# Kernel tuning notes

Measured on AMD Instinct MI355X. Metric: run time of the kernel, lower is better.

## Reference

```python
import jax, jax.numpy as jnp
import numpy as np

C = 16        # channel_n
HID = 128     # hidden width of 1x1 MLP
FIRE_RATE = 0.5
STEP_SIZE = 1.0
ALIVE_THRESH = 0.1
B, H, W = 16, 256, 256


def _perceive_kernel():
    # identity + Sobel filters, angle = 0.0 so cos=1, sin=0
    ident = np.outer([0.0, 1.0, 0.0], [0.0, 1.0, 0.0]).astype(np.float32)
    dxk = (np.outer([1.0, 2.0, 1.0], [-1.0, 0.0, 1.0]) / 8.0).astype(np.float32)
    dyk = dxk.T
    k3 = np.stack([ident, dxk, dyk], axis=-1)  # [3,3,3]
    # TF depthwise layout: out channel index = c*3 + k  -> tile over channels
    rhs = np.tile(k3, (1, 1, C)).reshape(3, 3, 1, 3 * C)  # HWIO, groups=C
    return jnp.asarray(rhs)


def _get_living_mask(x):
    alpha = x[:, :, :, 3:4]
    pooled = jax.lax.reduce_window(alpha, -jnp.inf, jax.lax.max,
                                   (1, 3, 3, 1), (1, 1, 1, 1), 'SAME')
    return pooled > ALIVE_THRESH


def _perceive(x):
    rhs = _perceive_kernel()
    return jax.lax.conv_general_dilated(
        x, rhs, window_strides=(1, 1), padding='SAME',
        dimension_numbers=('NHWC', 'HWIO', 'NHWC'),
        feature_group_count=C)  # [B,H,W,3C]


def setup_inputs() -> dict:
    key = jax.random.key(0)
    kx, kw1, kb1, ku = jax.random.split(key, 4)
    x = jax.random.normal(kx, (B, H, W, C), dtype=jnp.float32)
    # dmodel params: Conv2D(128,1,relu) then Conv2D(16,1,zeros init); use
    # random values for a meaningful numeric baseline
    W1 = jax.random.normal(kw1, (3 * C, HID), dtype=jnp.float32) * 0.1
    b1 = jax.random.normal(kb1, (HID,), dtype=jnp.float32) * 0.01
    W2 = jax.random.normal(jax.random.fold_in(key, 7), (HID, C), dtype=jnp.float32) * 0.1
    b2 = jnp.zeros((C,), dtype=jnp.float32)
    rand_u = jax.random.uniform(ku, (B, H, W, 1), dtype=jnp.float32)
    return {"x": x, "W1": W1, "b1": b1, "W2": W2, "b2": b2, "rand_u": rand_u}


def reference(x, W1, b1, W2, b2, rand_u):
    pre_life_mask = _get_living_mask(x)
    y = _perceive(x)                                         # [B,H,W,48]
    h = jax.nn.relu(jnp.einsum('bhwc,cd->bhwd', y, W1) + b1)  # [B,H,W,128]
    dx = (jnp.einsum('bhwd,dc->bhwc', h, W2) + b2) * STEP_SIZE
    update_mask = (rand_u <= FIRE_RATE).astype(x.dtype)
    x = x + dx * update_mask
    post_life_mask = _get_living_mask(x)
    life_mask = (pre_life_mask & post_life_mask).astype(x.dtype)
    return x * life_mask
```

## Files before the change

kernel.cpp:

```cpp
#include <hip/hip_runtime.h>


#define NC 16
#define NHID 128
#define NPIX (16 * 256 * 256)
#define MG 0.04f
#define MAXFIX 65536

typedef __attribute__((ext_vector_type(8))) short s8b;
typedef __attribute__((ext_vector_type(4))) float f4;

__device__ __forceinline__ unsigned short f2bf(float f) {
    union { float f; unsigned int u; } v; v.f = f;
    unsigned int r = (v.u + 0x7FFFu + ((v.u >> 16) & 1u)) >> 16;
    return (unsigned short)r;
}
__device__ __forceinline__ unsigned int pack2(float a, float b) {
    return (unsigned int)f2bf(a) | ((unsigned int)f2bf(b) << 16);
}

__global__ __launch_bounds__(256) void ca_prep(
    const float* __restrict__ W1, const float* __restrict__ b1,
    const float* __restrict__ W2, uint4* __restrict__ w1p, uint4* __restrict__ w2p)
{
    const int tid = threadIdx.x;
    if (blockIdx.x == 0) {
        for (int idx = tid; idx < 1024; idx += 256) {
            const int fid = idx >> 6, lane = idx & 63;
            const int k0 = fid >> 3, mt = fid & 7;
            const int q = lane >> 4, i = lane & 15;
            unsigned int u[4];
            #pragma unroll
            for (int jp = 0; jp < 4; ++jp) {
                int k = k0 * 32 + q * 8 + jp * 2;
                float v0 = (k < 48) ? W1[k * 128 + mt * 16 + i] : ((k == 48) ? b1[mt * 16 + i] : 0.f);
                k++;
                float v1 = (k < 48) ? W1[k * 128 + mt * 16 + i] : ((k == 48) ? b1[mt * 16 + i] : 0.f);
                u[jp] = pack2(v0, v1);
            }
            w1p[idx] = make_uint4(u[0], u[1], u[2], u[3]);
        }
    } else {
        for (int idx = tid; idx < 256; idx += 256) {
            const int k2 = idx >> 6, lane = idx & 63;
            const int q = lane >> 4, i = lane & 15;
            unsigned int u[4];
            #pragma unroll
            for (int jp = 0; jp < 4; ++jp) {
                const int k = k2 * 32 + q * 8 + jp * 2;
                u[jp] = pack2(W2[k * 16 + i], W2[(k + 1) * 16 + i]);
            }
            w2p[idx] = make_uint4(u[0], u[1], u[2], u[3]);
        }
    }
}

__global__ __launch_bounds__(256, 2) void ca_update(
    const float* __restrict__ x, const float* __restrict__ b2,
    const float* __restrict__ rand_u, const uint4* __restrict__ w1p,
    const uint4* __restrict__ w2p, float* __restrict__ out,
    float* __restrict__ ws_alpha, unsigned char* __restrict__ ws_pre,
    unsigned int* __restrict__ fix_cnt, unsigned int* __restrict__ fix_list)
{
    __shared__ __align__(16) float xt[18 * 18 * 20];
    __shared__ __align__(16) unsigned short yfs[4 * 2 * 528];
    __shared__ __align__(16) unsigned short hbs[4 * 16 * 136];
    __shared__ float lsr[256];

    const int tid  = threadIdx.x;
    const int lane = tid & 63;
    const int li   = lane & 15;
    const int lq   = lane >> 4;
    const int wv   = tid >> 6;
    const int tx   = tid & 15, ty = tid >> 4;
    const int w0 = blockIdx.x * 16, h0 = blockIdx.y * 16, bb = blockIdx.z;

    s8b w1f[2][8], w2f[4];
    const s8b* w1s = (const s8b*)w1p;
    const s8b* w2s = (const s8b*)w2p;
    #pragma unroll
    for (int k0 = 0; k0 < 2; ++k0)
        #pragma unroll
        for (int mt = 0; mt < 8; ++mt)
            w1f[k0][mt] = w1s[(k0 * 8 + mt) * 64 + lane];
    #pragma unroll
    for (int k2 = 0; k2 < 4; ++k2) w2f[k2] = w2s[k2 * 64 + lane];
    float b2v[4];
    #pragma unroll
    for (int r = 0; r < 4; ++r) b2v[r] = b2[lq * 4 + r];

    for (int i = tid; i < 324; i += 256) {
        const int ly = i / 18, lx = i - ly * 18;
        const int gh = h0 + ly - 1, gw = w0 + lx - 1;
        float4 v0, v1, v2, v3;
        if (gh >= 0 && gh < 256 && gw >= 0 && gw < 256) {
            const float4* p = (const float4*)(x + (((size_t)bb * 256 + gh) * 256 + gw) * NC);
            v0 = p[0]; v1 = p[1]; v2 = p[2]; v3 = p[3];
        } else {
            v0 = v1 = v2 = v3 = make_float4(0.f, 0.f, 0.f, 0.f);
        }
        float4* t = (float4*)(xt + i * 20);
        t[0] = v0; t[1] = v1; t[2] = v2; t[3] = v3;
    }
    const size_t gpix = ((size_t)bb * 256 + h0 + ty) * 256 + (w0 + tx);
    lsr[tid] = rand_u[gpix];
    __syncthreads();

    const int o_mm = ((ty + 0) * 18 + tx + 0) * 20, o_m0 = ((ty + 0) * 18 + tx + 1) * 20, o_mp = ((ty + 0) * 18 + tx + 2) * 20;
    const int o_0m = ((ty + 1) * 18 + tx + 0) * 20, o_cc = ((ty + 1) * 18 + tx + 1) * 20, o_0p = ((ty + 1) * 18 + tx + 2) * 20;
    const int o_pm = ((ty + 2) * 18 + tx + 0) * 20, o_p0 = ((ty + 2) * 18 + tx + 1) * 20, o_pp = ((ty + 2) * 18 + tx + 2) * 20;

    float am = xt[o_mm + 3];
    am = fmaxf(am, xt[o_m0 + 3]); am = fmaxf(am, xt[o_mp + 3]);
    am = fmaxf(am, xt[o_0m + 3]); am = fmaxf(am, xt[o_cc + 3]); am = fmaxf(am, xt[o_0p + 3]);
    am = fmaxf(am, xt[o_pm + 3]); am = fmaxf(am, xt[o_p0 + 3]); am = fmaxf(am, xt[o_pp + 3]);
    ws_pre[gpix] = (am > 0.1f) ? (unsigned char)1 : (unsigned char)0;

    unsigned int yu[24];
    #pragma unroll
    for (int cq = 0; cq < 4; ++cq) {
        const int co = cq * 4;
        float4 vmm = *(const float4*)(xt + o_mm + co); const float* pmm = (const float*)&vmm;
        float4 vm0 = *(const float4*)(xt + o_m0 + co); const float* pm0 = (const float*)&vm0;
        float4 vmp = *(const float4*)(xt + o_mp + co); const float* pmp = (const float*)&vmp;
        float4 v0m = *(const float4*)(xt + o_0m + co); const float* p0m = (const float*)&v0m;
        float4 vcc = *(const float4*)(xt + o_cc + co); const float* pcc = (const float*)&vcc;
        float4 v0p = *(const float4*)(xt + o_0p + co); const float* p0p = (const float*)&v0p;
        float4 vpm = *(const float4*)(xt + o_pm + co); const float* ppm = (const float*)&vpm;
        float4 vp0 = *(const float4*)(xt + o_p0 + co); const float* pp0 = (const float*)&vp0;
        float4 vpp = *(const float4*)(xt + o_pp + co); const float* ppp = (const float*)&vpp;
        float yl[12];
        #pragma unroll
        for (int cc = 0; cc < 4; ++cc) {
            const float xmm = pmm[cc], xm0 = pm0[cc], xmp = pmp[cc];
            const float x0m = p0m[cc], xcc = pcc[cc], x0p = p0p[cc];
            const float xpm = ppm[cc], xp0 = pp0[cc], xpp = ppp[cc];
            yl[cc * 3 + 0] = xcc;
            yl[cc * 3 + 1] = ((xmp - xmm) + 2.f * (x0p - x0m) + (xpp - xpm)) * 0.125f;
            yl[cc * 3 + 2] = ((xpm - xmm) + 2.f * (xp0 - xm0) + (xpp - xmp)) * 0.125f;
        }
        #pragma unroll
        for (int m2 = 0; m2 < 6; ++m2) yu[cq * 6 + m2] = pack2(yl[2 * m2], yl[2 * m2 + 1]);
    }

    unsigned short* yfw = yfs + wv * (2 * 528);
    unsigned short* hbw = hbs + wv * (16 * 136);

    for (int s = 0; s < 4; ++s) {
        const int t = wv * 4 + s;
        if ((ty & 3) == s) {
            #pragma unroll
            for (int q = 0; q < 4; ++q)
                *(uint4*)(yfw + (q * 16 + tx) * 8) = make_uint4(yu[q * 4], yu[q * 4 + 1], yu[q * 4 + 2], yu[q * 4 + 3]);
            *(uint4*)(yfw + 528 + (0 * 16 + tx) * 8) = make_uint4(yu[16], yu[17], yu[18], yu[19]);
            *(uint4*)(yfw + 528 + (1 * 16 + tx) * 8) = make_uint4(yu[20], yu[21], yu[22], yu[23]);
            *(uint4*)(yfw + 528 + (2 * 16 + tx) * 8) = make_uint4(0x3F80u, 0u, 0u, 0u);
            *(uint4*)(yfw + 528 + (3 * 16 + tx) * 8) = make_uint4(0u, 0u, 0u, 0u);
        }
        const s8b ya0 = *(const s8b*)(yfw + lane * 8);
        const s8b ya1 = *(const s8b*)(yfw + 528 + lane * 8);
        f4 acc1[8];
        #pragma unroll
        for (int mt = 0; mt < 8; ++mt) { f4 z = {0.f, 0.f, 0.f, 0.f}; acc1[mt] = z; }
        #pragma unroll
        for (int mt = 0; mt < 8; ++mt)
            acc1[mt] = __builtin_amdgcn_mfma_f32_16x16x32_bf16(w1f[0][mt], ya0, acc1[mt], 0, 0, 0);
        #pragma unroll
        for (int mt = 0; mt < 8; ++mt)
            acc1[mt] = __builtin_amdgcn_mfma_f32_16x16x32_bf16(w1f[1][mt], ya1, acc1[mt], 0, 0, 0);
        #pragma unroll
        for (int mt = 0; mt < 8; ++mt) {
            const float hh0 = fmaxf(acc1[mt][0], 0.f), hh1 = fmaxf(acc1[mt][1], 0.f);
            const float hh2 = fmaxf(acc1[mt][2], 0.f), hh3 = fmaxf(acc1[mt][3], 0.f);
            *(uint2*)(hbw + li * 136 + mt * 16 + lq * 4) = make_uint2(pack2(hh0, hh1), pack2(hh2, hh3));
        }
        f4 acc2 = {0.f, 0.f, 0.f, 0.f};
        #pragma unroll
        for (int k2 = 0; k2 < 4; ++k2) {
            const s8b hf = *(const s8b*)(hbw + li * 136 + k2 * 32 + lq * 8);
            acc2 = __builtin_amdgcn_mfma_f32_16x16x32_bf16(w2f[k2], hf, acc2, 0, 0, 0);
        }
        const float um = (lsr[t * 16 + li] <= 0.5f) ? 1.f : 0.f;
        const float4 xc = *(const float4*)(xt + ((t + 1) * 18 + li + 1) * 20 + lq * 4);
        float4 nx;
        nx.x = fmaf(acc2[0] + b2v[0], um, xc.x);
        nx.y = fmaf(acc2[1] + b2v[1], um, xc.y);
        nx.z = fmaf(acc2[2] + b2v[2], um, xc.z);
        nx.w = fmaf(acc2[3] + b2v[3], um, xc.w);
        const size_t gp = ((size_t)bb * 256 + h0 + t) * 256 + (w0 + li);
        ((float4*)out)[gp * 4 + lq] = nx;
        if (lq == 0) {
            ws_alpha[gp] = nx.w;
            if (um != 0.f && fabsf(nx.w - 0.1f) <= MG) {
                unsigned int idx = atomicAdd(fix_cnt, 1u);
                if (idx < MAXFIX) fix_list[idx] = (unsigned int)gp;
            }
        }
    }
}

__global__ __launch_bounds__(64) void ca_fix(
    const float* __restrict__ x, const float* __restrict__ W1,
    const float* __restrict__ b1, const float* __restrict__ W2,
    const float* __restrict__ b2,
    const unsigned int* __restrict__ fix_cnt, const unsigned int* __restrict__ fix_list,
    float* __restrict__ ws_alpha)
{
    __shared__ float ysh[48];
    const int lane = threadIdx.x;
    unsigned int n = *fix_cnt;
    if (n > MAXFIX) n = MAXFIX;
    for (unsigned int e = blockIdx.x; e < n; e += gridDim.x) {
        const unsigned int pix = fix_list[e];
        const int bb = pix >> 16, h = (pix >> 8) & 255, w = pix & 255;
        if (lane < 48) {
            const int c = lane / 3, j = lane - c * 3;
            float v = 0.f;
            #pragma unroll
            for (int dy = 0; dy < 3; ++dy) {
                #pragma unroll
                for (int dxx = 0; dxx < 3; ++dxx) {
                    const int hh = h + dy - 1, ww = w + dxx - 1;
                    if (hh < 0 || hh >= 256 || ww < 0 || ww >= 256) continue;
                    const float f = x[(((size_t)bb * 256 + hh) * 256 + ww) * 16 + c];
                    float wgt;
                    if (j == 0) wgt = (dy == 1 && dxx == 1) ? 1.f : 0.f;
                    else if (j == 1) wgt = ((dy == 1) ? 2.f : 1.f) * (float)(dxx - 1) * 0.125f;
                    else wgt = ((dxx == 1) ? 2.f : 1.f) * (float)(dy - 1) * 0.125f;
                    v = fmaf(f, wgt, v);
                }
            }
            ysh[lane] = v;
        }
        __syncthreads();
        float dot = 0.f;
        #pragma unroll
        for (int t = 0; t < 2; ++t) {
            const int d = t * 64 + lane;
            float a = b1[d];
            #pragma unroll
            for (int k = 0; k < 48; ++k)
                a = fmaf(ysh[k], W1[k * 128 + d], a);
            dot = fmaf(fmaxf(a, 0.f), W2[d * 16 + 3], dot);
        }
        #pragma unroll
        for (int off = 32; off > 0; off >>= 1)
            dot += __shfl_down(dot, off, 64);
        if (lane == 0)
            ws_alpha[pix] = x[(size_t)pix * 16 + 3] + dot + b2[3];
        __syncthreads();
    }
}

__global__ __launch_bounds__(256) void ca_mask(
    const float* __restrict__ alpha, const unsigned char* __restrict__ pre,
    float* __restrict__ out)
{
    __shared__ float at[18 * 20];
    const int tid = threadIdx.x;
    const int w0 = blockIdx.x * 16, h0 = blockIdx.y * 16, bb = blockIdx.z;
    for (int i = tid; i < 324; i += 256) {
        const int ly = i / 18, lx = i - ly * 18;
        const int gh = h0 + ly - 1, gw = w0 + lx - 1;
        float v = 0.f;
        if (gh >= 0 && gh < 256 && gw >= 0 && gw < 256)
            v = alpha[((size_t)bb * 256 + gh) * 256 + gw];
        at[ly * 20 + lx] = v;
    }
    __syncthreads();
    const int txx = tid & 15, tyy = tid >> 4;
    float m = at[tyy * 20 + txx];
    m = fmaxf(m, at[tyy * 20 + txx + 1]); m = fmaxf(m, at[tyy * 20 + txx + 2]);
    m = fmaxf(m, at[(tyy + 1) * 20 + txx]); m = fmaxf(m, at[(tyy + 1) * 20 + txx + 1]); m = fmaxf(m, at[(tyy + 1) * 20 + txx + 2]);
    m = fmaxf(m, at[(tyy + 2) * 20 + txx]); m = fmaxf(m, at[(tyy + 2) * 20 + txx + 1]); m = fmaxf(m, at[(tyy + 2) * 20 + txx + 2]);
    const size_t gp = ((size_t)bb * 256 + h0 + tyy) * 256 + (w0 + txx);
    const bool alive = (m > 0.1f) && pre[gp];
    if (!alive) {
        float4* po = (float4*)(out + gp * 16);
        const float4 z = make_float4(0.f, 0.f, 0.f, 0.f);
        po[0] = z; po[1] = z; po[2] = z; po[3] = z;
    }
}

extern "C" void kernel_launch(void* const* d_in, const int* in_sizes, int n_in,
                              void* d_out, int out_size, void* d_ws, size_t ws_size,
                              hipStream_t stream) {
    (void)in_sizes; (void)n_in; (void)out_size; (void)ws_size;
    const float* x  = (const float*)d_in[0];
    const float* W1 = (const float*)d_in[1];
    const float* b1 = (const float*)d_in[2];
    const float* W2 = (const float*)d_in[3];
    const float* b2 = (const float*)d_in[4];
    const float* ru = (const float*)d_in[5];
    float* out = (float*)d_out;

    char* ws = (char*)d_ws;
    float* ws_alpha       = (float*)ws;
    unsigned char* ws_pre = (unsigned char*)(ws + (size_t)NPIX * 4);
    uint4* w1p            = (uint4*)(ws + (size_t)NPIX * 5);
    uint4* w2p            = w1p + 1024;
    unsigned int* fix_cnt = (unsigned int*)(ws + (size_t)NPIX * 5 + 20480);
    unsigned int* fix_list= fix_cnt + 4;

    hipMemsetAsync(fix_cnt, 0, sizeof(unsigned int), stream);
    ca_prep<<<2, 256, 0, stream>>>(W1, b1, W2, w1p, w2p);
    dim3 g(16, 16, 16);
    ca_update<<<g, 256, 0, stream>>>(x, b2, ru, w1p, w2p, out, ws_alpha, ws_pre, fix_cnt, fix_list);
    ca_fix<<<4096, 64, 0, stream>>>(x, W1, b1, W2, b2, fix_cnt, fix_list, ws_alpha);
    ca_mask<<<g, 256, 0, stream>>>(ws_alpha, ws_pre, out);
}
```

Baseline: 332.8 us.

## Raise update occupancy by moving W2 fragments to LDS and slimming registers

The main update kernel raises its launch-bounds occupancy hint from 2 to 3 blocks per SM. It frees registers by keeping the W2 MFMA fragments in LDS instead of registers, and by building the constant bias/zero part of the second A operand in registers rather than storing it to LDS. The random-mask staging buffer is dropped in favour of direct per-row global loads, LDS strides are changed (likely to reduce bank conflicts), the weight prep is spread over more blocks, and the fix kernel now packs four wavefronts per block with no block barriers. The risks are extra LDS reads per MFMA step and possible register spills under the tighter bound.

Result: no change. 336.0 us (+1.0%).

```diff
diff --git a/kernel.cpp b/kernel.cpp
--- a/kernel.cpp
+++ b/kernel.cpp
@@ -23,39 +23,36 @@
     const float* __restrict__ W1, const float* __restrict__ b1,
     const float* __restrict__ W2, uint4* __restrict__ w1p, uint4* __restrict__ w2p)
 {
-    const int tid = threadIdx.x;
-    if (blockIdx.x == 0) {
-        for (int idx = tid; idx < 1024; idx += 256) {
-            const int fid = idx >> 6, lane = idx & 63;
-            const int k0 = fid >> 3, mt = fid & 7;
-            const int q = lane >> 4, i = lane & 15;
-            unsigned int u[4];
-            #pragma unroll
-            for (int jp = 0; jp < 4; ++jp) {
-                int k = k0 * 32 + q * 8 + jp * 2;
-                float v0 = (k < 48) ? W1[k * 128 + mt * 16 + i] : ((k == 48) ? b1[mt * 16 + i] : 0.f);
-                k++;
-                float v1 = (k < 48) ? W1[k * 128 + mt * 16 + i] : ((k == 48) ? b1[mt * 16 + i] : 0.f);
-                u[jp] = pack2(v0, v1);
-            }
-            w1p[idx] = make_uint4(u[0], u[1], u[2], u[3]);
-        }
-    } else {
-        for (int idx = tid; idx < 256; idx += 256) {
-            const int k2 = idx >> 6, lane = idx & 63;
-            const int q = lane >> 4, i = lane & 15;
-            unsigned int u[4];
-            #pragma unroll
-            for (int jp = 0; jp < 4; ++jp) {
-                const int k = k2 * 32 + q * 8 + jp * 2;
-                u[jp] = pack2(W2[k * 16 + i], W2[(k + 1) * 16 + i]);
-            }
-            w2p[idx] = make_uint4(u[0], u[1], u[2], u[3]);
-        }
-    }
-}
-
-__global__ __launch_bounds__(256, 2) void ca_update(
+    const int idx = blockIdx.x * 256 + threadIdx.x;
+    if (idx < 1024) {
+        const int fid = idx >> 6, lane = idx & 63;
+        const int k0 = fid >> 3, mt = fid & 7;
+        const int q = lane >> 4, i = lane & 15;
+        unsigned int u[4];
+        #pragma unroll
+        for (int jp = 0; jp < 4; ++jp) {
+            int k = k0 * 32 + q * 8 + jp * 2;
+            float v0 = (k < 48) ? W1[k * 128 + mt * 16 + i] : ((k == 48) ? b1[mt * 16 + i] : 0.f);
+            k++;
+            float v1 = (k < 48) ? W1[k * 128 + mt * 16 + i] : ((k == 48) ? b1[mt * 16 + i] : 0.f);
+            u[jp] = pack2(v0, v1);
+        }
+        w1p[idx] = make_uint4(u[0], u[1], u[2], u[3]);
+    } else if (idx < 1280) {
+        const int id2 = idx - 1024;
+        const int k2 = id2 >> 6, lane = id2 & 63;
+        const int q = lane >> 4, i = lane & 15;
+        unsigned int u[4];
+        #pragma unroll
+        for (int jp = 0; jp < 4; ++jp) {
+            const int k = k2 * 32 + q * 8 + jp * 2;
+            u[jp] = pack2(W2[k * 16 + i], W2[(k + 1) * 16 + i]);
+        }
+        w2p[id2] = make_uint4(u[0], u[1], u[2], u[3]);
+    }
+}
+
+__global__ __launch_bounds__(256, 3) void ca_update(
     const float* __restrict__ x, const float* __restrict__ b2,
     const float* __restrict__ rand_u, const uint4* __restrict__ w1p,
     const uint4* __restrict__ w2p, float* __restrict__ out,
@@ -63,9 +60,9 @@
     unsigned int* __restrict__ fix_cnt, unsigned int* __restrict__ fix_list)
 {
     __shared__ __align__(16) float xt[18 * 18 * 20];
-    __shared__ __align__(16) unsigned short yfs[4 * 2 * 528];
-    __shared__ __align__(16) unsigned short hbs[4 * 16 * 136];
-    __shared__ float lsr[256];
+    __shared__ __align__(16) unsigned char yfs[4 * 1536];
+    __shared__ __align__(16) unsigned char hbs[4 * 4224];
+    __shared__ __align__(16) uint4 w2L[256];
 
     const int tid  = threadIdx.x;
     const int lane = tid & 63;
@@ -75,16 +72,14 @@
     const int tx   = tid & 15, ty = tid >> 4;
     const int w0 = blockIdx.x * 16, h0 = blockIdx.y * 16, bb = blockIdx.z;
 
-    s8b w1f[2][8], w2f[4];
+    s8b w1f[2][8];
     const s8b* w1s = (const s8b*)w1p;
-    const s8b* w2s = (const s8b*)w2p;
     #pragma unroll
     for (int k0 = 0; k0 < 2; ++k0)
         #pragma unroll
         for (int mt = 0; mt < 8; ++mt)
             w1f[k0][mt] = w1s[(k0 * 8 + mt) * 64 + lane];
-    #pragma unroll
-    for (int k2 = 0; k2 < 4; ++k2) w2f[k2] = w2s[k2 * 64 + lane];
+    w2L[tid] = w2p[tid];
     float b2v[4];
     #pragma unroll
     for (int r = 0; r < 4; ++r) b2v[r] = b2[lq * 4 + r];
@@ -102,19 +97,20 @@
         float4* t = (float4*)(xt + i * 20);
         t[0] = v0; t[1] = v1; t[2] = v2; t[3] = v3;
     }
-    const size_t gpix = ((size_t)bb * 256 + h0 + ty) * 256 + (w0 + tx);
-    lsr[tid] = rand_u[gpix];
     __syncthreads();
 
     const int o_mm = ((ty + 0) * 18 + tx + 0) * 20, o_m0 = ((ty + 0) * 18 + tx + 1) * 20, o_mp = ((ty + 0) * 18 + tx + 2) * 20;
     const int o_0m = ((ty + 1) * 18 + tx + 0) * 20, o_cc = ((ty + 1) * 18 + tx + 1) * 20, o_0p = ((ty + 1) * 18 + tx + 2) * 20;
     const int o_pm = ((ty + 2) * 18 + tx + 0) * 20, o_p0 = ((ty + 2) * 18 + tx + 1) * 20, o_pp = ((ty + 2) * 18 + tx + 2) * 20;
 
-    float am = xt[o_mm + 3];
-    am = fmaxf(am, xt[o_m0 + 3]); am = fmaxf(am, xt[o_mp + 3]);
-    am = fmaxf(am, xt[o_0m + 3]); am = fmaxf(am, xt[o_cc + 3]); am = fmaxf(am, xt[o_0p + 3]);
-    am = fmaxf(am, xt[o_pm + 3]); am = fmaxf(am, xt[o_p0 + 3]); am = fmaxf(am, xt[o_pp + 3]);
-    ws_pre[gpix] = (am > 0.1f) ? (unsigned char)1 : (unsigned char)0;
+    {
+        float am = xt[o_mm + 3];
+        am = fmaxf(am, xt[o_m0 + 3]); am = fmaxf(am, xt[o_mp + 3]);
+        am = fmaxf(am, xt[o_0m + 3]); am = fmaxf(am, xt[o_cc + 3]); am = fmaxf(am, xt[o_0p + 3]);
+        am = fmaxf(am, xt[o_pm + 3]); am = fmaxf(am, xt[o_p0 + 3]); am = fmaxf(am, xt[o_pp + 3]);
+        const size_t gpix = ((size_t)bb * 256 + h0 + ty) * 256 + (w0 + tx);
+        ws_pre[gpix] = (am > 0.1f) ? (unsigned char)1 : (unsigned char)0;
+    }
 
     unsigned int yu[24];
     #pragma unroll
@@ -143,22 +139,25 @@
         for (int m2 = 0; m2 < 6; ++m2) yu[cq * 6 + m2] = pack2(yl[2 * m2], yl[2 * m2 + 1]);
     }
 
-    unsigned short* yfw = yfs + wv * (2 * 528);
-    unsigned short* hbw = hbs + wv * (16 * 136);
+    unsigned char* yfw = yfs + wv * 1536;
+    unsigned char* hbw = hbs + wv * 4224;
 
     for (int s = 0; s < 4; ++s) {
         const int t = wv * 4 + s;
         if ((ty & 3) == s) {
             #pragma unroll
             for (int q = 0; q < 4; ++q)
-                *(uint4*)(yfw + (q * 16 + tx) * 8) = make_uint4(yu[q * 4], yu[q * 4 + 1], yu[q * 4 + 2], yu[q * 4 + 3]);
-            *(uint4*)(yfw + 528 + (0 * 16 + tx) * 8) = make_uint4(yu[16], yu[17], yu[18], yu[19]);
-            *(uint4*)(yfw + 528 + (1 * 16 + tx) * 8) = make_uint4(yu[20], yu[21], yu[22], yu[23]);
-            *(uint4*)(yfw + 528 + (2 * 16 + tx) * 8) = make_uint4(0x3F80u, 0u, 0u, 0u);
-            *(uint4*)(yfw + 528 + (3 * 16 + tx) * 8) = make_uint4(0u, 0u, 0u, 0u);
-        }
-        const s8b ya0 = *(const s8b*)(yfw + lane * 8);
-        const s8b ya1 = *(const s8b*)(yfw + 528 + lane * 8);
+                *(uint4*)(yfw + (q * 16 + tx) * 16) = make_uint4(yu[q * 4], yu[q * 4 + 1], yu[q * 4 + 2], yu[q * 4 + 3]);
+            *(uint4*)(yfw + 1024 + tx * 16)       = make_uint4(yu[16], yu[17], yu[18], yu[19]);
+            *(uint4*)(yfw + 1024 + 256 + tx * 16) = make_uint4(yu[20], yu[21], yu[22], yu[23]);
+        }
+        const s8b ya0 = *(const s8b*)(yfw + lane * 16);
+        s8b ya1;
+        {
+            s8b z = {0, 0, 0, 0, 0, 0, 0, 0};
+            if (lane < 32) ya1 = *(const s8b*)(yfw + 1024 + lane * 16);
+            else { z[0] = (lq == 2) ? (short)0x3F80 : (short)0; ya1 = z; }
+        }
         f4 acc1[8];
         #pragma unroll
         for (int mt = 0; mt < 8; ++mt) { f4 z = {0.f, 0.f, 0.f, 0.f}; acc1[mt] = z; }
@@ -172,22 +171,25 @@
         for (int mt = 0; mt < 8; ++mt) {
             const float hh0 = fmaxf(acc1[mt][0], 0.f), hh1 = fmaxf(acc1[mt][1], 0.f);
             const float hh2 = fmaxf(acc1[mt][2], 0.f), hh3 = fmaxf(acc1[mt][3], 0.f);
-            *(uint2*)(hbw + li * 136 + mt * 16 + lq * 4) = make_uint2(pack2(hh0, hh1), pack2(hh2, hh3));
+            *(uint2*)(hbw + li * 264 + mt * 32 + lq * 8) = make_uint2(pack2(hh0, hh1), pack2(hh2, hh3));
         }
         f4 acc2 = {0.f, 0.f, 0.f, 0.f};
         #pragma unroll
         for (int k2 = 0; k2 < 4; ++k2) {
-            const s8b hf = *(const s8b*)(hbw + li * 136 + k2 * 32 + lq * 8);
-            acc2 = __builtin_amdgcn_mfma_f32_16x16x32_bf16(w2f[k2], hf, acc2, 0, 0, 0);
-        }
-        const float um = (lsr[t * 16 + li] <= 0.5f) ? 1.f : 0.f;
+            const s8b hf  = *(const s8b*)(hbw + li * 264 + k2 * 64 + lq * 16);
+            const s8b w2f = *(const s8b*)((const unsigned char*)w2L + (k2 * 64 + lane) * 16);
+            acc2 = __builtin_amdgcn_mfma_f32_16x16x32_bf16(w2f, hf, acc2, 0, 0, 0);
+        }
+        const size_t grow = ((size_t)bb * 256 + h0 + t) * 256 + w0;
+        const float rv = rand_u[grow + li];
+        const float um = (rv <= 0.5f) ? 1.f : 0.f;
         const float4 xc = *(const float4*)(xt + ((t + 1) * 18 + li + 1) * 20 + lq * 4);
         float4 nx;
         nx.x = fmaf(acc2[0] + b2v[0], um, xc.x);
         nx.y = fmaf(acc2[1] + b2v[1], um, xc.y);
         nx.z = fmaf(acc2[2] + b2v[2], um, xc.z);
         nx.w = fmaf(acc2[3] + b2v[3], um, xc.w);
-        const size_t gp = ((size_t)bb * 256 + h0 + t) * 256 + (w0 + li);
+        const size_t gp = grow + li;
         ((float4*)out)[gp * 4 + lq] = nx;
         if (lq == 0) {
             ws_alpha[gp] = nx.w;
@@ -199,18 +201,18 @@
     }
 }
 
-__global__ __launch_bounds__(64) void ca_fix(
+__global__ __launch_bounds__(256) void ca_fix(
     const float* __restrict__ x, const float* __restrict__ W1,
     const float* __restrict__ b1, const float* __restrict__ W2,
     const float* __restrict__ b2,
     const unsigned int* __restrict__ fix_cnt, const unsigned int* __restrict__ fix_list,
     float* __restrict__ ws_alpha)
 {
-    __shared__ float ysh[48];
-    const int lane = threadIdx.x;
+    __shared__ float ysh[4][64];
+    const int wv = threadIdx.x >> 6, lane = threadIdx.x & 63;
     unsigned int n = *fix_cnt;
     if (n > MAXFIX) n = MAXFIX;
-    for (unsigned int e = blockIdx.x; e < n; e += gridDim.x) {
+    for (unsigned int e = blockIdx.x * 4 + wv; e < n; e += gridDim.x * 4) {
         const unsigned int pix = fix_list[e];
         const int bb = pix >> 16, h = (pix >> 8) & 255, w = pix & 255;
         if (lane < 48) {
@@ -230,9 +232,8 @@
                     v = fmaf(f, wgt, v);
                 }
             }
-            ysh[lane] = v;
-        }
-        __syncthreads();
+            ysh[wv][lane] = v;
+        }
         float dot = 0.f;
         #pragma unroll
         for (int t = 0; t < 2; ++t) {
@@ -240,7 +241,7 @@
             float a = b1[d];
             #pragma unroll
             for (int k = 0; k < 48; ++k)
-                a = fmaf(ysh[k], W1[k * 128 + d], a);
+                a = fmaf(ysh[wv][k], W1[k * 128 + d], a);
             dot = fmaf(fmaxf(a, 0.f), W2[d * 16 + 3], dot);
         }
         #pragma unroll
@@ -248,7 +249,6 @@
             dot += __shfl_down(dot, off, 64);
         if (lane == 0)
             ws_alpha[pix] = x[(size_t)pix * 16 + 3] + dot + b2[3];
-        __syncthreads();
     }
 }
 
@@ -303,9 +303,9 @@
     unsigned int* fix_list= fix_cnt + 4;
 
     hipMemsetAsync(fix_cnt, 0, sizeof(unsigned int), stream);
-    ca_prep<<<2, 256, 0, stream>>>(W1, b1, W2, w1p, w2p);
+    ca_prep<<<5, 256, 0, stream>>>(W1, b1, W2, w1p, w2p);
     dim3 g(16, 16, 16);
     ca_update<<<g, 256, 0, stream>>>(x, b2, ru, w1p, w2p, out, ws_alpha, ws_pre, fix_cnt, fix_list);
-    ca_fix<<<4096, 64, 0, stream>>>(x, W1, b1, W2, b2, fix_cnt, fix_list, ws_alpha);
+    ca_fix<<<512, 256, 0, stream>>>(x, W1, b1, W2, b2, fix_cnt, fix_list, ws_alpha);
     ca_mask<<<g, 256, 0, stream>>>(ws_alpha, ws_pre, out);
 }
```
